# Kernel optimization log

Hardware: AMD Instinct MI355X
Metric: run time of the kernel (lower is better)

## Reference

```python
import jax, jax.numpy as jnp
import numpy as np

EPS = 1e-5

def _layernorm(x, g, b):
    m = jnp.mean(x, axis=-1, keepdims=True)
    v = jnp.mean((x - m) ** 2, axis=-1, keepdims=True)
    return (x - m) * jax.lax.rsqrt(v + EPS) * g + b

def setup_inputs() -> dict:
    key = jax.random.key(0)
    ks = jax.random.split(key, 6)
    b, s, n = 1, 256, 512
    dim_msa, dim_pair, heads, dim_head = 64, 128, 8, 32
    dim_inner = heads * dim_head
    msa = jax.random.normal(ks[0], (b, s, n, dim_msa), dtype=jnp.float32)
    pairwise_repr = jax.random.normal(ks[1], (b, n, n, dim_pair), dtype=jnp.float32)
    mask = jnp.ones((b, n), dtype=bool)
    return {
        "msa": msa,
        "pairwise_repr": pairwise_repr,
        "ln_msa_g": jnp.ones((dim_msa,), jnp.float32),
        "ln_msa_b": jnp.zeros((dim_msa,), jnp.float32),
        "W_vg": jax.random.normal(ks[2], (dim_msa, dim_inner * 2), jnp.float32) * 0.02,
        "ln_pair_g": jnp.ones((dim_pair,), jnp.float32),
        "ln_pair_b": jnp.zeros((dim_pair,), jnp.float32),
        "W_pair": jax.random.normal(ks[3], (dim_pair, heads), jnp.float32) * 0.02,
        "W_out": jax.random.normal(ks[4], (dim_inner, dim_msa), jnp.float32) * 0.02,
        "mask": mask,
    }

def reference(msa, pairwise_repr, ln_msa_g, ln_msa_b, W_vg, ln_pair_g, ln_pair_b, W_pair, W_out, mask):
    heads, dim_head = 8, 32
    b, s, n, dim_msa = msa.shape
    # values and gates: LN -> LinearNoBias -> split (gv h d)
    vg = _layernorm(msa, ln_msa_g, ln_msa_b) @ W_vg            # [b,s,n,2*h*d]
    vg = vg.reshape(b, s, n, 2, heads, dim_head)
    vg = jnp.transpose(vg, (3, 0, 4, 1, 2, 5))                  # [2,b,h,s,n,d]
    values, gates = vg[0], jax.nn.sigmoid(vg[1])
    # pair bias: LN -> LinearNoBias -> [b,h,i,j]
    bias = _layernorm(pairwise_repr, ln_pair_g, ln_pair_b) @ W_pair  # [b,i,j,h]
    bias = jnp.transpose(bias, (0, 3, 1, 2))                    # [b,h,i,j]
    bias = jnp.where(mask[:, None, None, :], bias, -jnp.inf)
    weights = jax.nn.softmax(bias, axis=-1)                     # [b,h,i,j]
    out = jnp.einsum('bhij,bhsjd->bhsid', weights, values)      # [b,h,s,n,d]
    out = out * gates
    out = jnp.transpose(out, (0, 2, 3, 1, 4)).reshape(b, s, n, heads * dim_head)
    return out @ W_out                                          # [b,s,n,dim_msa]
```

## Files before the change

### kernel.cpp

```cpp
#include <hip/hip_runtime.h>
#include <hip/hip_bf16.h>


#define S 256
#define N 512
#define DM 64
#define DP 128
#define H 8
#define C 256
#define ROWS (S * N)

typedef __attribute__((ext_vector_type(8))) short bf16x8;
typedef __attribute__((ext_vector_type(4))) float f32x4;

static __device__ __forceinline__ float bf2f(unsigned int u16) {
    union { unsigned int i; float f; } x;
    x.i = u16 << 16;
    return x.f;
}
static __device__ __forceinline__ unsigned short f2bf(float f) {
    union { float f; unsigned int i; } x;
    x.f = f;
    unsigned int r = x.i + 0x7FFFu + ((x.i >> 16) & 1u);
    return (unsigned short)(r >> 16);
}
static __device__ __forceinline__ void gload16(const void* g, void* l) {
    __builtin_amdgcn_global_load_lds(
        (const __attribute__((address_space(1))) void*)g,
        (__attribute__((address_space(3))) void*)l, 16, 0, 0);
}

__global__ __launch_bounds__(256) void k0_prep(
    const float* __restrict__ Wvg, const float* __restrict__ g, const float* __restrict__ b,
    const float* __restrict__ Wout, const float* __restrict__ gp, const float* __restrict__ bp,
    const float* __restrict__ Wp,
    unsigned short* __restrict__ WTvg, float* __restrict__ biasvg, unsigned short* __restrict__ WoutT,
    float* __restrict__ Wg, float* __restrict__ sgcb)
{
    const int t = threadIdx.x;
    if (blockIdx.x < 2) {
        const int c = blockIdx.x * 256 + t;
        float bias = 0.f;
        unsigned short row[64];
#pragma unroll
        for (int k = 0; k < 64; k++) {
            const float w = Wvg[k * 512 + c];
            row[k] = f2bf(w * g[k]);
            bias = fmaf(w, b[k], bias);
        }
#pragma unroll
        for (int q = 0; q < 8; q++) *(uint4*)(WTvg + c * 64 + q * 8) = *(const uint4*)(row + q * 8);
        biasvg[c] = bias;
    } else if (blockIdx.x == 2) {
        const int m = t >> 2, c0 = (t & 3) * 64;
        unsigned short row[64];
#pragma unroll
        for (int q = 0; q < 64; q++) row[q] = f2bf(Wout[(c0 + q) * 64 + m]);
#pragma unroll
        for (int q = 0; q < 8; q++) *(uint4*)(WoutT + m * 256 + c0 + q * 8) = *(const uint4*)(row + q * 8);
    } else {
        if (t < 128) {
            const float gm = gp[t];
#pragma unroll
            for (int h = 0; h < 8; h++) Wg[t * 8 + h] = gm * Wp[t * 8 + h];
        } else if (t < 136) {
            const int h = t - 128;
            float sg = 0.f, cb = 0.f;
            for (int k = 0; k < 128; k++) {
                sg = fmaf(gp[k], Wp[k * 8 + h], sg);
                cb = fmaf(bp[k], Wp[k * 8 + h], cb);
            }
            sgcb[h] = sg;
            sgcb[8 + h] = cb;
        }
    }
}

__global__ __launch_bounds__(512) void k12_fused(
    const float* __restrict__ msa, const unsigned short* __restrict__ WTvg,
    const float* __restrict__ biasvg,
    unsigned short* __restrict__ VT, unsigned short* __restrict__ G,
    const float* __restrict__ pair, const float* __restrict__ Wg,
    const float* __restrict__ sgcb, unsigned short* __restrict__ Wt)
{
    __shared__ __align__(16) char smem[16384];
    const int t = threadIdx.x;

    if ((blockIdx.x & 1) == 0) {
        float (*bias_lds)[N] = (float(*)[N])smem;
        const int i = blockIdx.x >> 1;
        const int sub = t & 15, rgrp = t >> 4;

        float wreg[2][4][8];
#pragma unroll
        for (int q = 0; q < 2; q++)
#pragma unroll
            for (int c = 0; c < 4; c++) {
                const int k = (q * 16 + sub) * 4 + c;
                const float4 w0 = *(const float4*)(Wg + k * 8);
                const float4 w1 = *(const float4*)(Wg + k * 8 + 4);
                wreg[q][c][0] = w0.x; wreg[q][c][1] = w0.y; wreg[q][c][2] = w0.z; wreg[q][c][3] = w0.w;
                wreg[q][c][4] = w1.x; wreg[q][c][5] = w1.y; wreg[q][c][6] = w1.z; wreg[q][c][7] = w1.w;
            }
        float sgr[8], cbr[8];
#pragma unroll
        for (int h = 0; h < 8; h++) { sgr[h] = sgcb[h]; cbr[h] = sgcb[8 + h]; }

        for (int pass = 0; pass < 16; ++pass) {
            const int r = pass * 32 + rgrp;
            const float* px = pair + ((size_t)i * N + r) * DP;
            const float4 x0 = *(const float4*)(px + sub * 4);
            const float4 x1 = *(const float4*)(px + 64 + sub * 4);
            float s1 = x0.x + x0.y + x0.z + x0.w + x1.x + x1.y + x1.z + x1.w;
            float s2 = x0.x * x0.x + x0.y * x0.y + x0.z * x0.z + x0.w * x0.w
                     + x1.x * x1.x + x1.y * x1.y + x1.z * x1.z + x1.w * x1.w;
#pragma unroll
            for (int off = 1; off < 16; off <<= 1) {
                s1 += __shfl_xor(s1, off);
                s2 += __shfl_xor(s2, off);
            }
            const float m = s1 * (1.f / 128.f);
            const float inv = rsqrtf(s2 * (1.f / 128.f) - m * m + 1e-5f);

            float dots[8];
#pragma unroll
            for (int h = 0; h < 8; h++) dots[h] = 0.f;
            const float xs[2][4] = {{x0.x, x0.y, x0.z, x0.w}, {x1.x, x1.y, x1.z, x1.w}};
#pragma unroll
            for (int q = 0; q < 2; q++)
#pragma unroll
                for (int c = 0; c < 4; c++)
#pragma unroll
                    for (int h = 0; h < 8; h++) dots[h] = fmaf(xs[q][c], wreg[q][c][h], dots[h]);
#pragma unroll
            for (int off = 1; off < 16; off <<= 1)
#pragma unroll
                for (int h = 0; h < 8; h++) dots[h] += __shfl_xor(dots[h], off);

            if (sub == 0) {
#pragma unroll
                for (int h = 0; h < 8; h++)
                    bias_lds[h][r] = inv * (dots[h] - m * sgr[h]) + cbr[h];
            }
        }
        __syncthreads();

        const int lane = t & 63, h = t >> 6;
        float v[8];
        float mx = -1e30f;
#pragma unroll
        for (int q = 0; q < 8; q++) {
            v[q] = bias_lds[h][q * 64 + lane];
            mx = fmaxf(mx, v[q]);
        }
#pragma unroll
        for (int off = 32; off > 0; off >>= 1) mx = fmaxf(mx, __shfl_xor(mx, off));
        float sum = 0.f;
#pragma unroll
        for (int q = 0; q < 8; q++) {
            v[q] = __expf(v[q] - mx);
            sum += v[q];
        }
#pragma unroll
        for (int off = 32; off > 0; off >>= 1) sum += __shfl_xor(sum, off);
        const float rs = 1.f / sum;
#pragma unroll
        for (int q = 0; q < 8; q++)
            Wt[((size_t)h * N + i) * N + q * 64 + lane] = f2bf(v[q] * rs);
    } else {
        unsigned short* at = (unsigned short*)smem;
        const int bid1 = blockIdx.x >> 1;
        const int lane = t & 63, w = t >> 6;
        const int l15 = lane & 15, lgrp = lane >> 4;
        const int s = bid1 >> 1;
        const int jbase = (bid1 & 1) * 256;

        bf16x8 bfr[4][2];
#pragma unroll
        for (int cf = 0; cf < 4; cf++)
#pragma unroll
            for (int ks = 0; ks < 2; ks++) {
                const int c = w * 64 + cf * 16 + l15;
                bfr[cf][ks] = *(const bf16x8*)(WTvg + c * 64 + ks * 32 + lgrp * 8);
            }
        float biasr[4];
        float bias2[4][4];
        if (w < 4) {
#pragma unroll
            for (int cf = 0; cf < 4; cf++) biasr[cf] = biasvg[w * 64 + cf * 16 + l15];
        } else {
#pragma unroll
            for (int cf = 0; cf < 4; cf++)
#pragma unroll
                for (int r = 0; r < 4; r++) bias2[cf][r] = biasvg[w * 64 + cf * 16 + lgrp * 4 + r];
        }

        for (int tile = 0; tile < 4; ++tile) {
            const int j0 = jbase + tile * 64;
            {
                const int r = t >> 3, kc = (t & 7) * 8;
                const float* src = msa + ((size_t)(s * 512 + j0 + r)) * 64 + kc;
                const float4 x0 = *(const float4*)src;
                const float4 x1 = *(const float4*)(src + 4);
                float s1 = x0.x + x0.y + x0.z + x0.w + x1.x + x1.y + x1.z + x1.w;
                float s2 = x0.x * x0.x + x0.y * x0.y + x0.z * x0.z + x0.w * x0.w
                         + x1.x * x1.x + x1.y * x1.y + x1.z * x1.z + x1.w * x1.w;
#pragma unroll
                for (int off = 1; off < 8; off <<= 1) {
                    s1 += __shfl_xor(s1, off);
                    s2 += __shfl_xor(s2, off);
                }
                const float m = s1 * (1.f / 64.f);
                const float inv = rsqrtf(s2 * (1.f / 64.f) - m * m + 1e-5f);
                unsigned short buf[8];
                buf[0] = f2bf((x0.x - m) * inv); buf[1] = f2bf((x0.y - m) * inv);
                buf[2] = f2bf((x0.z - m) * inv); buf[3] = f2bf((x0.w - m) * inv);
                buf[4] = f2bf((x1.x - m) * inv); buf[5] = f2bf((x1.y - m) * inv);
                buf[6] = f2bf((x1.z - m) * inv); buf[7] = f2bf((x1.w - m) * inv);
                *(uint4*)((char*)at + r * 128 + (((t & 7) ^ (r & 7)) * 16)) = *(const uint4*)buf;
            }
            __syncthreads();

            f32x4 acc[4][4];
#pragma unroll
            for (int rf = 0; rf < 4; rf++)
#pragma unroll
                for (int cf = 0; cf < 4; cf++) acc[rf][cf] = (f32x4){0.f, 0.f, 0.f, 0.f};

#pragma unroll
            for (int ks = 0; ks < 2; ks++) {
#pragma unroll
                for (int rf = 0; rf < 4; rf++) {
                    const int rr = rf * 16 + l15;
                    const bf16x8 afr = *(const bf16x8*)((const char*)at + rr * 128 + (((ks * 4 + lgrp) ^ (rr & 7)) * 16));
                    if (w < 4) {
#pragma unroll
                        for (int cf = 0; cf < 4; cf++)
                            acc[rf][cf] = __builtin_amdgcn_mfma_f32_16x16x32_bf16(afr, bfr[cf][ks], acc[rf][cf], 0, 0, 0);
                    } else {
#pragma unroll
                        for (int cf = 0; cf < 4; cf++)
                            acc[rf][cf] = __builtin_amdgcn_mfma_f32_16x16x32_bf16(bfr[cf][ks], afr, acc[rf][cf], 0, 0, 0);
                    }
                }
            }
            __syncthreads();

            if (w < 4) {
#pragma unroll
                for (int rf = 0; rf < 4; rf++)
#pragma unroll
                    for (int cf = 0; cf < 4; cf++) {
                        const int c = w * 64 + cf * 16 + l15;
                        const int j = j0 + rf * 16 + lgrp * 4;
                        uint2 o;
                        o.x = (unsigned)f2bf(acc[rf][cf][0] + biasr[cf]) |
                              ((unsigned)f2bf(acc[rf][cf][1] + biasr[cf]) << 16);
                        o.y = (unsigned)f2bf(acc[rf][cf][2] + biasr[cf]) |
                              ((unsigned)f2bf(acc[rf][cf][3] + biasr[cf]) << 16);
                        *(uint2*)(VT + ((size_t)s * C + c) * N + j) = o;
                    }
            } else {
#pragma unroll
                for (int rf = 0; rf < 4; rf++)
#pragma unroll
                    for (int cf = 0; cf < 4; cf++) {
                        const int j = j0 + rf * 16 + l15;
                        const int cp = (w - 4) * 64 + cf * 16 + lgrp * 4;
                        float sg[4];
#pragma unroll
                        for (int r = 0; r < 4; r++)
                            sg[r] = 1.f / (1.f + __expf(-(acc[rf][cf][r] + bias2[cf][r])));
                        uint2 o;
                        o.x = (unsigned)f2bf(sg[0]) | ((unsigned)f2bf(sg[1]) << 16);
                        o.y = (unsigned)f2bf(sg[2]) | ((unsigned)f2bf(sg[3]) << 16);
                        *(uint2*)(G + ((size_t)(s * 512 + j)) * C + cp) = o;
                    }
            }
        }
    }
}

__global__ __launch_bounds__(256, 2) void k3_fused_out(
    const unsigned short* __restrict__ Wt, const unsigned short* __restrict__ VT,
    const unsigned short* __restrict__ G, const unsigned short* __restrict__ WoutT,
    float* __restrict__ out)
{
    __shared__ unsigned short a_lds[64 * 64];
    __shared__ unsigned short b_lds[128 * 64];
    __shared__ unsigned short g_lds[2 * 128 * 32];
    const int raw = blockIdx.x;
    const int bid = (raw & 7) * 64 + (raw >> 3);
    const int sp = bid >> 2;
    const int it = bid & 3;
    const int s0 = sp * 2, i0 = it * 128;
    const int t = threadIdx.x, lane = t & 63, w = t >> 6;
    const int l15 = lane & 15, lgrp = lane >> 4;
    const int wn = w >> 1, wi = w & 1;

    const unsigned short* srcA[2];
    const unsigned short* srcB[4];
    int dstA[2], dstB[4];
#pragma unroll
    for (int q = 0; q < 2; ++q) {
        const int slot = q * 256 + t;
        const int row = slot >> 3, chp = slot & 7;
        const int ch = chp ^ (row & 7);
        srcA[q] = VT + ((size_t)((s0 + (row >> 5)) * 256 + (row & 31))) * 512 + ch * 8;
        dstA[q] = slot * 16;
    }
#pragma unroll
    for (int q = 0; q < 4; ++q) {
        const int slot = q * 256 + t;
        const int row = slot >> 3, chp = slot & 7;
        const int ch = chp ^ (row & 7);
        srcB[q] = Wt + ((size_t)(i0 + row)) * 512 + ch * 8;
        dstB[q] = slot * 16;
    }

    f32x4 oacc[2][2][4];
#pragma unroll
    for (int s = 0; s < 2; s++)
#pragma unroll
        for (int f = 0; f < 2; f++)
#pragma unroll
            for (int mf = 0; mf < 4; mf++) oacc[s][f][mf] = (f32x4){0.f, 0.f, 0.f, 0.f};

    for (int h = 0; h < 8; ++h) {
        uint2 gpre[2][4];
#pragma unroll
        for (int fn = 0; fn < 2; ++fn)
#pragma unroll
            for (int fi = 0; fi < 4; ++fi)
                gpre[fn][fi] = *(const uint2*)(G +
                    ((size_t)((s0 + wn) * 512 + i0 + wi * 64 + fi * 16 + l15)) * 256 +
                    h * 32 + fn * 16 + lgrp * 4);

        f32x4 acc[2][4];
#pragma unroll
        for (int fn = 0; fn < 2; fn++)
#pragma unroll
            for (int fi = 0; fi < 4; fi++) acc[fn][fi] = (f32x4){0.f, 0.f, 0.f, 0.f};

        const int offA = h * 16384;
        const int offB = h * 262144;
        for (int kt = 0; kt < 8; ++kt) {
            const int j0 = kt * 64;
#pragma unroll
            for (int q = 0; q < 2; ++q) gload16(srcA[q] + offA + j0, (char*)a_lds + dstA[q]);
#pragma unroll
            for (int q = 0; q < 4; ++q) gload16(srcB[q] + offB + j0, (char*)b_lds + dstB[q]);
            __syncthreads();
#pragma unroll
            for (int ks = 0; ks < 2; ++ks) {
                bf16x8 af[2], bf[4];
#pragma unroll
                for (int fn = 0; fn < 2; ++fn) {
                    const int ra = wn * 32 + fn * 16 + l15;
                    af[fn] = *(const bf16x8*)((const char*)a_lds + ra * 128 + (((ks * 4 + lgrp) ^ (ra & 7)) * 16));
                }
#pragma unroll
                for (int fi = 0; fi < 4; ++fi) {
                    const int rb = wi * 64 + fi * 16 + l15;
                    bf[fi] = *(const bf16x8*)((const char*)b_lds + rb * 128 + (((ks * 4 + lgrp) ^ (rb & 7)) * 16));
                }
#pragma unroll
                for (int fn = 0; fn < 2; ++fn)
#pragma unroll
                    for (int fi = 0; fi < 4; ++fi)
                        acc[fn][fi] = __builtin_amdgcn_mfma_f32_16x16x32_bf16(af[fn], bf[fi], acc[fn][fi], 0, 0, 0);
            }
            __syncthreads();
        }

#pragma unroll
        for (int fn = 0; fn < 2; ++fn) {
            const int d0 = fn * 16 + lgrp * 4;
#pragma unroll
            for (int fi = 0; fi < 4; ++fi) {
                const int i = wi * 64 + fi * 16 + l15;
                const uint2 uu = gpre[fn][fi];
                const float g0 = bf2f(uu.x & 0xFFFFu), g1 = bf2f(uu.x >> 16);
                const float g2 = bf2f(uu.y & 0xFFFFu), g3 = bf2f(uu.y >> 16);
                uint2 o;
                o.x = (unsigned)f2bf(acc[fn][fi][0] * g0) | ((unsigned)f2bf(acc[fn][fi][1] * g1) << 16);
                o.y = (unsigned)f2bf(acc[fn][fi][2] * g2) | ((unsigned)f2bf(acc[fn][fi][3] * g3) << 16);
                *(uint2*)((char*)g_lds + wn * 8192 + i * 64 + (((d0 >> 3) ^ (i & 3)) * 16) + (d0 & 7) * 2) = o;
            }
        }
        __syncthreads();

        bf16x8 bw[4];
#pragma unroll
        for (int mf = 0; mf < 4; ++mf)
            bw[mf] = *(const bf16x8*)(WoutT + (mf * 16 + l15) * 256 + h * 32 + lgrp * 8);
#pragma unroll
        for (int s = 0; s < 2; ++s) {
#pragma unroll
            for (int f = 0; f < 2; ++f) {
                const int ra = w * 32 + f * 16 + l15;
                const bf16x8 af = *(const bf16x8*)((const char*)g_lds + s * 8192 + ra * 64 + ((lgrp ^ (ra & 3)) * 16));
#pragma unroll
                for (int mf = 0; mf < 4; ++mf)
                    oacc[s][f][mf] = __builtin_amdgcn_mfma_f32_16x16x32_bf16(af, bw[mf], oacc[s][f][mf], 0, 0, 0);
            }
        }
        __syncthreads();
    }

#pragma unroll
    for (int s = 0; s < 2; ++s)
#pragma unroll
        for (int f = 0; f < 2; ++f)
#pragma unroll
            for (int mf = 0; mf < 4; ++mf)
#pragma unroll
                for (int r = 0; r < 4; ++r) {
                    const size_t row = (size_t)(s0 + s) * 512 + i0 + w * 32 + f * 16 + lgrp * 4 + r;
                    out[row * 64 + mf * 16 + l15] = oacc[s][f][mf][r];
                }
}

extern "C" void kernel_launch(void* const* d_in, const int* in_sizes, int n_in,
                              void* d_out, int out_size, void* d_ws, size_t ws_size,
                              hipStream_t stream) {
    (void)in_sizes; (void)n_in; (void)out_size; (void)ws_size;
    const float* msa       = (const float*)d_in[0];
    const float* pair      = (const float*)d_in[1];
    const float* ln_msa_g  = (const float*)d_in[2];
    const float* ln_msa_b  = (const float*)d_in[3];
    const float* W_vg      = (const float*)d_in[4];
    const float* ln_pair_g = (const float*)d_in[5];
    const float* ln_pair_b = (const float*)d_in[6];
    const float* W_pair    = (const float*)d_in[7];
    const float* W_out     = (const float*)d_in[8];
    float* out = (float*)d_out;

    char* ws = (char*)d_ws;
    size_t off = 0;
    unsigned short* VT    = (unsigned short*)(ws + off); off += (size_t)ROWS * C * 2;
    unsigned short* G     = (unsigned short*)(ws + off); off += (size_t)ROWS * C * 2;
    unsigned short* Wt    = (unsigned short*)(ws + off); off += (size_t)H * N * N * 2;
    unsigned short* WTvg  = (unsigned short*)(ws + off); off += 512 * 64 * 2;
    float*          biasvg = (float*)(ws + off); off += 512 * 4;
    unsigned short* WoutT = (unsigned short*)(ws + off); off += 64 * 256 * 2;
    float*          Wg    = (float*)(ws + off); off += 128 * 8 * 4;
    float*          sgcb  = (float*)(ws + off); off += 16 * 4;

    k0_prep<<<4, 256, 0, stream>>>(W_vg, ln_msa_g, ln_msa_b, W_out, ln_pair_g, ln_pair_b, W_pair,
                                   WTvg, biasvg, WoutT, Wg, sgcb);
    k12_fused<<<1024, 512, 0, stream>>>(msa, WTvg, biasvg, VT, G, pair, Wg, sgcb, Wt);
    k3_fused_out<<<512, 256, 0, stream>>>(Wt, VT, G, WoutT, out);
}
```

Measured before the change: 204.8 us.

## Split fused bias/VG kernel into separate pair-bias, softmax, and VG MFMA kernels

Replaces the single heterogeneous kernel, whose even blocks computed pair bias plus softmax and whose odd blocks computed the VG projection, with three kernels. The pair-bias LayerNorm-projection now runs over 2048 smaller blocks and writes a bf16 [i,j,h] intermediate. A separate softmax kernel reads that intermediate, and the VG MFMA kernel gets its own launch with a higher occupancy hint. This targets load imbalance between the two block types and the low parallelism of the bias path. In exchange it adds two kernel launches, an extra global round trip for the bias buffer, and rounds the bias to bf16 before the softmax.

```diff
diff --git a/kernel.cpp b/kernel.cpp
--- a/kernel.cpp
+++ b/kernel.cpp
@@ -76,209 +76,215 @@
     }
 }
 
-__global__ __launch_bounds__(512) void k12_fused(
+__global__ __launch_bounds__(512, 4) void k1_vg_mfma(
     const float* __restrict__ msa, const unsigned short* __restrict__ WTvg,
     const float* __restrict__ biasvg,
-    unsigned short* __restrict__ VT, unsigned short* __restrict__ G,
-    const float* __restrict__ pair, const float* __restrict__ Wg,
-    const float* __restrict__ sgcb, unsigned short* __restrict__ Wt)
+    unsigned short* __restrict__ VT, unsigned short* __restrict__ G)
 {
-    __shared__ __align__(16) char smem[16384];
-    const int t = threadIdx.x;
-
-    if ((blockIdx.x & 1) == 0) {
-        float (*bias_lds)[N] = (float(*)[N])smem;
-        const int i = blockIdx.x >> 1;
-        const int sub = t & 15, rgrp = t >> 4;
-
-        float wreg[2][4][8];
-#pragma unroll
-        for (int q = 0; q < 2; q++)
-#pragma unroll
-            for (int c = 0; c < 4; c++) {
-                const int k = (q * 16 + sub) * 4 + c;
-                const float4 w0 = *(const float4*)(Wg + k * 8);
-                const float4 w1 = *(const float4*)(Wg + k * 8 + 4);
-                wreg[q][c][0] = w0.x; wreg[q][c][1] = w0.y; wreg[q][c][2] = w0.z; wreg[q][c][3] = w0.w;
-                wreg[q][c][4] = w1.x; wreg[q][c][5] = w1.y; wreg[q][c][6] = w1.z; wreg[q][c][7] = w1.w;
-            }
-        float sgr[8], cbr[8];
-#pragma unroll
-        for (int h = 0; h < 8; h++) { sgr[h] = sgcb[h]; cbr[h] = sgcb[8 + h]; }
-
-        for (int pass = 0; pass < 16; ++pass) {
-            const int r = pass * 32 + rgrp;
-            const float* px = pair + ((size_t)i * N + r) * DP;
-            const float4 x0 = *(const float4*)(px + sub * 4);
-            const float4 x1 = *(const float4*)(px + 64 + sub * 4);
+    __shared__ unsigned short at[64 * 64];
+    const int t = threadIdx.x, lane = t & 63, w = t >> 6;
+    const int l15 = lane & 15, lgrp = lane >> 4;
+    const int s = blockIdx.x >> 1;
+    const int jbase = (blockIdx.x & 1) * 256;
+
+    bf16x8 bfr[4][2];
+#pragma unroll
+    for (int cf = 0; cf < 4; cf++)
+#pragma unroll
+        for (int ks = 0; ks < 2; ks++) {
+            const int c = w * 64 + cf * 16 + l15;
+            bfr[cf][ks] = *(const bf16x8*)(WTvg + c * 64 + ks * 32 + lgrp * 8);
+        }
+    float biasr[4];
+    float bias2[4][4];
+    if (w < 4) {
+#pragma unroll
+        for (int cf = 0; cf < 4; cf++) biasr[cf] = biasvg[w * 64 + cf * 16 + l15];
+    } else {
+#pragma unroll
+        for (int cf = 0; cf < 4; cf++)
+#pragma unroll
+            for (int r = 0; r < 4; r++) bias2[cf][r] = biasvg[w * 64 + cf * 16 + lgrp * 4 + r];
+    }
+
+    for (int tile = 0; tile < 4; ++tile) {
+        const int j0 = jbase + tile * 64;
+        {
+            const int r = t >> 3, kc = (t & 7) * 8;
+            const float* src = msa + ((size_t)(s * 512 + j0 + r)) * 64 + kc;
+            const float4 x0 = *(const float4*)src;
+            const float4 x1 = *(const float4*)(src + 4);
             float s1 = x0.x + x0.y + x0.z + x0.w + x1.x + x1.y + x1.z + x1.w;
             float s2 = x0.x * x0.x + x0.y * x0.y + x0.z * x0.z + x0.w * x0.w
                      + x1.x * x1.x + x1.y * x1.y + x1.z * x1.z + x1.w * x1.w;
 #pragma unroll
-            for (int off = 1; off < 16; off <<= 1) {
+            for (int off = 1; off < 8; off <<= 1) {
                 s1 += __shfl_xor(s1, off);
                 s2 += __shfl_xor(s2, off);
             }
-            const float m = s1 * (1.f / 128.f);
-            const float inv = rsqrtf(s2 * (1.f / 128.f) - m * m + 1e-5f);
-
-            float dots[8];
-#pragma unroll
-            for (int h = 0; h < 8; h++) dots[h] = 0.f;
-            const float xs[2][4] = {{x0.x, x0.y, x0.z, x0.w}, {x1.x, x1.y, x1.z, x1.w}};
-#pragma unroll
-            for (int q = 0; q < 2; q++)
-#pragma unroll
-                for (int c = 0; c < 4; c++)
-#pragma unroll
-                    for (int h = 0; h < 8; h++) dots[h] = fmaf(xs[q][c], wreg[q][c][h], dots[h]);
-#pragma unroll
-            for (int off = 1; off < 16; off <<= 1)
-#pragma unroll
-                for (int h = 0; h < 8; h++) dots[h] += __shfl_xor(dots[h], off);
-
-            if (sub == 0) {
-#pragma unroll
-                for (int h = 0; h < 8; h++)
-                    bias_lds[h][r] = inv * (dots[h] - m * sgr[h]) + cbr[h];
-            }
+            const float m = s1 * (1.f / 64.f);
+            const float inv = rsqrtf(s2 * (1.f / 64.f) - m * m + 1e-5f);
+            unsigned short buf[8];
+            buf[0] = f2bf((x0.x - m) * inv); buf[1] = f2bf((x0.y - m) * inv);
+            buf[2] = f2bf((x0.z - m) * inv); buf[3] = f2bf((x0.w - m) * inv);
+            buf[4] = f2bf((x1.x - m) * inv); buf[5] = f2bf((x1.y - m) * inv);
+            buf[6] = f2bf((x1.z - m) * inv); buf[7] = f2bf((x1.w - m) * inv);
+            *(uint4*)((char*)at + r * 128 + (((t & 7) ^ (r & 7)) * 16)) = *(const uint4*)buf;
         }
         __syncthreads();
 
-        const int lane = t & 63, h = t >> 6;
-        float v[8];
-        float mx = -1e30f;
-#pragma unroll
-        for (int q = 0; q < 8; q++) {
-            v[q] = bias_lds[h][q * 64 + lane];
-            mx = fmaxf(mx, v[q]);
-        }
-#pragma unroll
-        for (int off = 32; off > 0; off >>= 1) mx = fmaxf(mx, __shfl_xor(mx, off));
-        float sum = 0.f;
-#pragma unroll
-        for (int q = 0; q < 8; q++) {
-            v[q] = __expf(v[q] - mx);
-            sum += v[q];
-        }
-#pragma unroll
-        for (int off = 32; off > 0; off >>= 1) sum += __shfl_xor(sum, off);
-        const float rs = 1.f / sum;
-#pragma unroll
-        for (int q = 0; q < 8; q++)
-            Wt[((size_t)h * N + i) * N + q * 64 + lane] = f2bf(v[q] * rs);
-    } else {
-        unsigned short* at = (unsigned short*)smem;
-        const int bid1 = blockIdx.x >> 1;
-        const int lane = t & 63, w = t >> 6;
-        const int l15 = lane & 15, lgrp = lane >> 4;
-        const int s = bid1 >> 1;
-        const int jbase = (bid1 & 1) * 256;
-
-        bf16x8 bfr[4][2];
-#pragma unroll
-        for (int cf = 0; cf < 4; cf++)
-#pragma unroll
-            for (int ks = 0; ks < 2; ks++) {
-                const int c = w * 64 + cf * 16 + l15;
-                bfr[cf][ks] = *(const bf16x8*)(WTvg + c * 64 + ks * 32 + lgrp * 8);
-            }
-        float biasr[4];
-        float bias2[4][4];
+        f32x4 acc[4][4];
+#pragma unroll
+        for (int rf = 0; rf < 4; rf++)
+#pragma unroll
+            for (int cf = 0; cf < 4; cf++) acc[rf][cf] = (f32x4){0.f, 0.f, 0.f, 0.f};
+
+#pragma unroll
+        for (int ks = 0; ks < 2; ks++) {
+#pragma unroll
+            for (int rf = 0; rf < 4; rf++) {
+                const int rr = rf * 16 + l15;
+                const bf16x8 afr = *(const bf16x8*)((const char*)at + rr * 128 + (((ks * 4 + lgrp) ^ (rr & 7)) * 16));
+                if (w < 4) {
+#pragma unroll
+                    for (int cf = 0; cf < 4; cf++)
+                        acc[rf][cf] = __builtin_amdgcn_mfma_f32_16x16x32_bf16(afr, bfr[cf][ks], acc[rf][cf], 0, 0, 0);
+                } else {
+#pragma unroll
+                    for (int cf = 0; cf < 4; cf++)
+                        acc[rf][cf] = __builtin_amdgcn_mfma_f32_16x16x32_bf16(bfr[cf][ks], afr, acc[rf][cf], 0, 0, 0);
+                }
+            }
+        }
+        __syncthreads();
+
         if (w < 4) {
 #pragma unroll
-            for (int cf = 0; cf < 4; cf++) biasr[cf] = biasvg[w * 64 + cf * 16 + l15];
+            for (int rf = 0; rf < 4; rf++)
+#pragma unroll
+                for (int cf = 0; cf < 4; cf++) {
+                    const int c = w * 64 + cf * 16 + l15;
+                    const int j = j0 + rf * 16 + lgrp * 4;
+                    uint2 o;
+                    o.x = (unsigned)f2bf(acc[rf][cf][0] + biasr[cf]) |
+                          ((unsigned)f2bf(acc[rf][cf][1] + biasr[cf]) << 16);
+                    o.y = (unsigned)f2bf(acc[rf][cf][2] + biasr[cf]) |
+                          ((unsigned)f2bf(acc[rf][cf][3] + biasr[cf]) << 16);
+                    *(uint2*)(VT + ((size_t)s * C + c) * N + j) = o;
+                }
         } else {
 #pragma unroll
-            for (int cf = 0; cf < 4; cf++)
-#pragma unroll
-                for (int r = 0; r < 4; r++) bias2[cf][r] = biasvg[w * 64 + cf * 16 + lgrp * 4 + r];
-        }
-
-        for (int tile = 0; tile < 4; ++tile) {
-            const int j0 = jbase + tile * 64;
-            {
-                const int r = t >> 3, kc = (t & 7) * 8;
-                const float* src = msa + ((size_t)(s * 512 + j0 + r)) * 64 + kc;
-                const float4 x0 = *(const float4*)src;
-                const float4 x1 = *(const float4*)(src + 4);
-                float s1 = x0.x + x0.y + x0.z + x0.w + x1.x + x1.y + x1.z + x1.w;
-                float s2 = x0.x * x0.x + x0.y * x0.y + x0.z * x0.z + x0.w * x0.w
-                         + x1.x * x1.x + x1.y * x1.y + x1.z * x1.z + x1.w * x1.w;
-#pragma unroll
-                for (int off = 1; off < 8; off <<= 1) {
-                    s1 += __shfl_xor(s1, off);
-                    s2 += __shfl_xor(s2, off);
-                }
-                const float m = s1 * (1.f / 64.f);
-                const float inv = rsqrtf(s2 * (1.f / 64.f) - m * m + 1e-5f);
-                unsigned short buf[8];
-                buf[0] = f2bf((x0.x - m) * inv); buf[1] = f2bf((x0.y - m) * inv);
-                buf[2] = f2bf((x0.z - m) * inv); buf[3] = f2bf((x0.w - m) * inv);
-                buf[4] = f2bf((x1.x - m) * inv); buf[5] = f2bf((x1.y - m) * inv);
-                buf[6] = f2bf((x1.z - m) * inv); buf[7] = f2bf((x1.w - m) * inv);
-                *(uint4*)((char*)at + r * 128 + (((t & 7) ^ (r & 7)) * 16)) = *(const uint4*)buf;
-            }
-            __syncthreads();
-
-            f32x4 acc[4][4];
-#pragma unroll
             for (int rf = 0; rf < 4; rf++)
 #pragma unroll
-                for (int cf = 0; cf < 4; cf++) acc[rf][cf] = (f32x4){0.f, 0.f, 0.f, 0.f};
-
-#pragma unroll
-            for (int ks = 0; ks < 2; ks++) {
-#pragma unroll
-                for (int rf = 0; rf < 4; rf++) {
-                    const int rr = rf * 16 + l15;
-                    const bf16x8 afr = *(const bf16x8*)((const char*)at + rr * 128 + (((ks * 4 + lgrp) ^ (rr & 7)) * 16));
-                    if (w < 4) {
-#pragma unroll
-                        for (int cf = 0; cf < 4; cf++)
-                            acc[rf][cf] = __builtin_amdgcn_mfma_f32_16x16x32_bf16(afr, bfr[cf][ks], acc[rf][cf], 0, 0, 0);
-                    } else {
-#pragma unroll
-                        for (int cf = 0; cf < 4; cf++)
-                            acc[rf][cf] = __builtin_amdgcn_mfma_f32_16x16x32_bf16(bfr[cf][ks], afr, acc[rf][cf], 0, 0, 0);
-                    }
-                }
-            }
-            __syncthreads();
-
-            if (w < 4) {
-#pragma unroll
-                for (int rf = 0; rf < 4; rf++)
-#pragma unroll
-                    for (int cf = 0; cf < 4; cf++) {
-                        const int c = w * 64 + cf * 16 + l15;
-                        const int j = j0 + rf * 16 + lgrp * 4;
-                        uint2 o;
-                        o.x = (unsigned)f2bf(acc[rf][cf][0] + biasr[cf]) |
-                              ((unsigned)f2bf(acc[rf][cf][1] + biasr[cf]) << 16);
-                        o.y = (unsigned)f2bf(acc[rf][cf][2] + biasr[cf]) |
-                              ((unsigned)f2bf(acc[rf][cf][3] + biasr[cf]) << 16);
-                        *(uint2*)(VT + ((size_t)s * C + c) * N + j) = o;
-                    }
-            } else {
-#pragma unroll
-                for (int rf = 0; rf < 4; rf++)
-#pragma unroll
-                    for (int cf = 0; cf < 4; cf++) {
-                        const int j = j0 + rf * 16 + l15;
-                        const int cp = (w - 4) * 64 + cf * 16 + lgrp * 4;
-                        float sg[4];
-#pragma unroll
-                        for (int r = 0; r < 4; r++)
-                            sg[r] = 1.f / (1.f + __expf(-(acc[rf][cf][r] + bias2[cf][r])));
-                        uint2 o;
-                        o.x = (unsigned)f2bf(sg[0]) | ((unsigned)f2bf(sg[1]) << 16);
-                        o.y = (unsigned)f2bf(sg[2]) | ((unsigned)f2bf(sg[3]) << 16);
-                        *(uint2*)(G + ((size_t)(s * 512 + j)) * C + cp) = o;
-                    }
-            }
-        }
-    }
+                for (int cf = 0; cf < 4; cf++) {
+                    const int j = j0 + rf * 16 + l15;
+                    const int cp = (w - 4) * 64 + cf * 16 + lgrp * 4;
+                    float sg[4];
+#pragma unroll
+                    for (int r = 0; r < 4; r++)
+                        sg[r] = 1.f / (1.f + __expf(-(acc[rf][cf][r] + bias2[cf][r])));
+                    uint2 o;
+                    o.x = (unsigned)f2bf(sg[0]) | ((unsigned)f2bf(sg[1]) << 16);
+                    o.y = (unsigned)f2bf(sg[2]) | ((unsigned)f2bf(sg[3]) << 16);
+                    *(uint2*)(G + ((size_t)(s * 512 + j)) * C + cp) = o;
+                }
+        }
+    }
+}
+
+__global__ __launch_bounds__(256) void k2a_bias(
+    const float* __restrict__ pair, const float* __restrict__ Wg,
+    const float* __restrict__ sgcb, unsigned short* __restrict__ biasb)
+{
+    const int i = blockIdx.x >> 2;
+    const int jq = blockIdx.x & 3;
+    const int t = threadIdx.x;
+    const int sub = t & 15, rgrp = t >> 4;
+
+    float wreg[2][4][8];
+#pragma unroll
+    for (int q = 0; q < 2; q++)
+#pragma unroll
+        for (int c = 0; c < 4; c++) {
+            const int k = (q * 16 + sub) * 4 + c;
+            const float4 w0 = *(const float4*)(Wg + k * 8);
+            const float4 w1 = *(const float4*)(Wg + k * 8 + 4);
+            wreg[q][c][0] = w0.x; wreg[q][c][1] = w0.y; wreg[q][c][2] = w0.z; wreg[q][c][3] = w0.w;
+            wreg[q][c][4] = w1.x; wreg[q][c][5] = w1.y; wreg[q][c][6] = w1.z; wreg[q][c][7] = w1.w;
+        }
+    float sgr[8], cbr[8];
+#pragma unroll
+    for (int h = 0; h < 8; h++) { sgr[h] = sgcb[h]; cbr[h] = sgcb[8 + h]; }
+
+#pragma unroll
+    for (int pass = 0; pass < 8; ++pass) {
+        const int j = jq * 128 + pass * 16 + rgrp;
+        const float* px = pair + ((size_t)i * N + j) * DP;
+        const float4 x0 = *(const float4*)(px + sub * 4);
+        const float4 x1 = *(const float4*)(px + 64 + sub * 4);
+        float s1 = x0.x + x0.y + x0.z + x0.w + x1.x + x1.y + x1.z + x1.w;
+        float s2 = x0.x * x0.x + x0.y * x0.y + x0.z * x0.z + x0.w * x0.w
+                 + x1.x * x1.x + x1.y * x1.y + x1.z * x1.z + x1.w * x1.w;
+#pragma unroll
+        for (int off = 1; off < 16; off <<= 1) {
+            s1 += __shfl_xor(s1, off);
+            s2 += __shfl_xor(s2, off);
+        }
+        const float m = s1 * (1.f / 128.f);
+        const float inv = rsqrtf(s2 * (1.f / 128.f) - m * m + 1e-5f);
+
+        float dots[8];
+#pragma unroll
+        for (int h = 0; h < 8; h++) dots[h] = 0.f;
+        const float xs[2][4] = {{x0.x, x0.y, x0.z, x0.w}, {x1.x, x1.y, x1.z, x1.w}};
+#pragma unroll
+        for (int q = 0; q < 2; q++)
+#pragma unroll
+            for (int c = 0; c < 4; c++)
+#pragma unroll
+                for (int h = 0; h < 8; h++) dots[h] = fmaf(xs[q][c], wreg[q][c][h], dots[h]);
+#pragma unroll
+        for (int off = 1; off < 16; off <<= 1)
+#pragma unroll
+            for (int h = 0; h < 8; h++) dots[h] += __shfl_xor(dots[h], off);
+
+        if (sub == 0) {
+            unsigned short b8[8];
+#pragma unroll
+            for (int h = 0; h < 8; h++)
+                b8[h] = f2bf(inv * (dots[h] - m * sgr[h]) + cbr[h]);
+            *(uint4*)(biasb + ((size_t)i * N + j) * 8) = *(const uint4*)b8;
+        }
+    }
+}
+
+__global__ __launch_bounds__(512) void k2b_softmax(
+    const unsigned short* __restrict__ biasb, unsigned short* __restrict__ Wt)
+{
+    const int i = blockIdx.x;
+    const int t = threadIdx.x, lane = t & 63, h = t >> 6;
+
+    float v[8];
+    float mx = -1e30f;
+#pragma unroll
+    for (int q = 0; q < 8; q++) {
+        v[q] = bf2f(biasb[((size_t)i * N + q * 64 + lane) * 8 + h]);
+        mx = fmaxf(mx, v[q]);
+    }
+#pragma unroll
+    for (int off = 32; off > 0; off >>= 1) mx = fmaxf(mx, __shfl_xor(mx, off));
+    float sum = 0.f;
+#pragma unroll
+    for (int q = 0; q < 8; q++) {
+        v[q] = __expf(v[q] - mx);
+        sum += v[q];
+    }
+#pragma unroll
+    for (int off = 32; off > 0; off >>= 1) sum += __shfl_xor(sum, off);
+    const float rs = 1.f / sum;
+#pragma unroll
+    for (int q = 0; q < 8; q++)
+        Wt[((size_t)h * N + i) * N + q * 64 + lane] = f2bf(v[q] * rs);
 }
 
 __global__ __launch_bounds__(256, 2) void k3_fused_out(
@@ -441,6 +447,7 @@
     unsigned short* VT    = (unsigned short*)(ws + off); off += (size_t)ROWS * C * 2;
     unsigned short* G     = (unsigned short*)(ws + off); off += (size_t)ROWS * C * 2;
     unsigned short* Wt    = (unsigned short*)(ws + off); off += (size_t)H * N * N * 2;
+    unsigned short* biasb = (unsigned short*)(ws + off); off += (size_t)N * N * 8 * 2;
     unsigned short* WTvg  = (unsigned short*)(ws + off); off += 512 * 64 * 2;
     float*          biasvg = (float*)(ws + off); off += 512 * 4;
     unsigned short* WoutT = (unsigned short*)(ws + off); off += 64 * 256 * 2;
@@ -449,6 +456,8 @@
 
     k0_prep<<<4, 256, 0, stream>>>(W_vg, ln_msa_g, ln_msa_b, W_out, ln_pair_g, ln_pair_b, W_pair,
                                    WTvg, biasvg, WoutT, Wg, sgcb);
-    k12_fused<<<1024, 512, 0, stream>>>(msa, WTvg, biasvg, VT, G, pair, Wg, sgcb, Wt);
+    k2a_bias<<<2048, 256, 0, stream>>>(pair, Wg, sgcb, biasb);
+    k2b_softmax<<<512, 512, 0, stream>>>(biasb, Wt);
+    k1_vg_mfma<<<512, 512, 0, stream>>>(msa, WTvg, biasvg, VT, G);
     k3_fused_out<<<512, 256, 0, stream>>>(Wt, VT, G, WoutT, out);
 }
```

Result: slower. 233.7 us (+14.1%).
